# Kernel tuning notes

Measured on AMD Instinct MI355X. Metric: run time of the kernel, lower is better.

The kernel has to match this reference:

```python
import jax, jax.numpy as jnp
import numpy as np
from jax import lax

B, E, V, T = 16384, 256, 128, 16
TAU = 1.0


def _gru(x, h, Wih, Whh, bih, bhh):
    # torch.nn.GRUCell math
    gi = x @ Wih.T + bih
    gh = h @ Whh.T + bhh
    ir, iz, i_n = jnp.split(gi, 3, axis=-1)
    hr, hz, h_n = jnp.split(gh, 3, axis=-1)
    r = jax.nn.sigmoid(ir + hr)
    z = jax.nn.sigmoid(iz + hz)
    n = jnp.tanh(i_n + r * h_n)
    return (1.0 - z) * n + z * h


def setup_inputs() -> dict:
    key = jax.random.key(0)
    ks = jax.random.split(key, 10)
    s = 0.05
    w = lambda k, shape: jax.random.normal(k, shape, jnp.float32) * s
    return {
        "x": jax.random.normal(ks[0], (B, E), jnp.float32),
        "global_idxes": jnp.arange(B, dtype=jnp.int32),
        "uniform_noise": jax.random.uniform(ks[1], (T, B, V), dtype=jnp.float32),
        "dec_Wd2e": w(ks[2], (E, V)), "dec_bd2e": jnp.zeros((E,), jnp.float32),
        "dec_Wih": w(ks[3], (3 * E, E)), "dec_Whh": w(ks[4], (3 * E, E)),
        "dec_bih": jnp.zeros((3 * E,), jnp.float32), "dec_bhh": jnp.zeros((3 * E,), jnp.float32),
        "dec_We2d": w(ks[5], (V, E)), "dec_be2d": jnp.zeros((V,), jnp.float32),
        "enc_Wd2e": w(ks[6], (E, V)), "enc_bd2e": jnp.zeros((E,), jnp.float32),
        "enc_Wih": w(ks[7], (3 * E, E)), "enc_Whh": w(ks[8], (3 * E, E)),
        "enc_bih": jnp.zeros((3 * E,), jnp.float32), "enc_bhh": jnp.zeros((3 * E,), jnp.float32),
    }


def _forward(x, uniform_noise,
             dec_Wd2e, dec_bd2e, dec_Wih, dec_Whh, dec_bih, dec_bhh, dec_We2d, dec_be2d,
             enc_Wd2e, enc_bd2e, enc_Wih, enc_Whh, enc_bih, enc_bhh):
    Bn = x.shape[0]
    # gumbel noise from pre-sampled uniforms (deterministic)
    gnoise = -jnp.log(-jnp.log(uniform_noise + 1e-10) + 1e-10)  # [T,B,V]

    # ---- GumbelDecoder: sequential GRUCell decode with alive/dead masking ----
    def dec_step(carry, g_t):
        state, last_tok, alive, N, t = carry
        emb = last_tok @ dec_Wd2e.T + dec_bd2e
        state = _gru(emb, state, dec_Wih, dec_Whh, dec_bih, dec_bhh)
        logits = state @ dec_We2d.T + dec_be2d
        y_soft = jax.nn.softmax((logits + g_t) / TAU, axis=-1)
        idx = jnp.argmax(y_soft, axis=-1)
        y_hard = jax.nn.one_hot(idx, V, dtype=y_soft.dtype)
        # straight-through hard gumbel-softmax
        y = y_soft + lax.stop_gradient(y_hard - y_soft)
        ended = idx == 0  # token 0 is the terminator
        N = jnp.where(ended, jnp.minimum(N, t), N)
        alive = alive & (~ended)
        # dead rows (incl. newly ended) have their token zeroed, as in torch
        y = jnp.where(alive[:, None], y, 0.0)
        return (state, y, alive, N, t + 1), y

    init = (x, jnp.zeros((Bn, V), x.dtype), jnp.ones((Bn,), bool),
            jnp.full((Bn,), T, jnp.int32), jnp.int32(0))
    (_, _, _, N, _), utt = lax.scan(dec_step, init, gnoise)  # utt: [T,B,V]

    # ---- OnehotEncoder: sequential GRUCell encode with alive sieve (masked) ----
    def enc_step(carry, u_t):
        state, out_state, alive = carry
        emb = u_t @ enc_Wd2e.T + enc_bd2e
        state = _gru(emb, state, enc_Wih, enc_Whh, enc_bih, enc_bhh)
        out_state = jnp.where(alive[:, None], state, out_state)
        ended = u_t[:, 0] > 0.5  # terminator seen in utterance
        alive = alive & (~ended)
        return (state, out_state, alive), None

    z0 = jnp.zeros((Bn, E), x.dtype)
    (_, reconst, _), _ = lax.scan(enc_step, (z0, z0, jnp.ones((Bn,), bool)), utt)

    utterance = jnp.transpose(utt, (1, 0, 2))  # [B,T,V]
    return utterance, N, reconst


def reference(x, global_idxes, uniform_noise,
              dec_Wd2e, dec_bd2e, dec_Wih, dec_Whh, dec_bih, dec_bhh, dec_We2d, dec_be2d,
              enc_Wd2e, enc_bd2e, enc_Wih, enc_Whh, enc_bih, enc_bhh):
    del global_idxes  # unused by the original forward
    return _forward(x, uniform_noise,
                    dec_Wd2e, dec_bd2e, dec_Wih, dec_Whh, dec_bih, dec_bhh, dec_We2d, dec_be2d,
                    enc_Wd2e, enc_bd2e, enc_Wih, enc_Whh, enc_bih, enc_bhh)
```

## Files before the change

### kernel.cpp

```cpp
#include <hip/hip_runtime.h>


namespace {
constexpr int kB  = 16384;
constexpr int kE  = 256;
constexpr int kV  = 128;
constexpr int kT  = 16;
constexpr int kG3 = 768;

constexpr int kOffWdhhT  = 0;
constexpr int kOffWe2dT  = kG3 * kE;
constexpr int kOffDecTab = kOffWe2dT + kV * kE;
constexpr int kOffEncTab = kOffDecTab + 129 * kG3;
constexpr int kOffBTab   = kOffEncTab + 129 * kG3;
constexpr int kBCount    = 32 * kG3 * 8;
}

typedef short bf16x8 __attribute__((ext_vector_type(8)));
typedef float f32x4  __attribute__((ext_vector_type(4)));
typedef unsigned short u16;

__device__ __forceinline__ float sigmf(float v) { return 1.0f / (1.0f + expf(-v)); }
__device__ __forceinline__ float gumbelf(float u) {
  return -logf(-logf(u + 1e-10f) + 1e-10f);
}

__device__ __forceinline__ f32x4 mfma16(bf16x8 a, bf16x8 b, f32x4 c) {
  return __builtin_amdgcn_mfma_f32_16x16x32_bf16(a, b, c, 0, 0, 0);
}

struct Bf3 { bf16x8 h, m, l; };

__device__ __forceinline__ Bf3 split3(float4 a, float4 b) {
  const float v[8] = {a.x, a.y, a.z, a.w, b.x, b.y, b.z, b.w};
  union { bf16x8 b8; u16 u[8]; } H, M, L;
#pragma unroll
  for (int e = 0; e < 8; ++e) {
    const float f = v[e];
    const unsigned hb = __float_as_uint(f) & 0xffff0000u;
    const float f1 = f - __uint_as_float(hb);
    const unsigned mb = __float_as_uint(f1) & 0xffff0000u;
    const float f2 = f1 - __uint_as_float(mb);
    H.u[e] = (u16)(hb >> 16);
    M.u[e] = (u16)(mb >> 16);
    L.u[e] = (u16)(__float_as_uint(f2) >> 16);
  }
  Bf3 r; r.h = H.b8; r.m = M.b8; r.l = L.b8;
  return r;
}

__device__ __forceinline__ int hidx(int row, int col) {
  return row * kE + ((((col >> 3) ^ (row & 7)) << 3) | (col & 7));
}

__global__ void prep_transpose(const float* __restrict__ dWhh,
                               const float* __restrict__ We2d,
                               float* __restrict__ ws) {
  const int n1 = kG3 * kE;
  const int n2 = n1 + kV * kE;
  for (int i = blockIdx.x * blockDim.x + threadIdx.x; i < n2;
       i += gridDim.x * blockDim.x) {
    if (i < n1) {
      const int k = i / kG3, j = i - k * kG3;
      ws[i] = dWhh[j * kE + k];
    } else {
      const int t = i - n1;
      const int k = t / kV, v = t - k * kV;
      ws[i] = We2d[v * kE + k];
    }
  }
}

__global__ void prep_tables(const float* __restrict__ Wih,
                            const float* __restrict__ Wd2e,
                            const float* __restrict__ bd2e,
                            const float* __restrict__ bih,
                            float* __restrict__ tab) {
  const int i = blockIdx.x * blockDim.x + threadIdx.x;
  if (i >= 129 * kG3) return;
  const int v = i / kG3, j = i - v * kG3;
  const float* wr = Wih + j * kE;
  float acc = 0.0f;
  if (v < kV) {
    for (int k = 0; k < kE; ++k) acc = fmaf(wr[k], Wd2e[k * kV + v] + bd2e[k], acc);
  } else {
    for (int k = 0; k < kE; ++k) acc = fmaf(wr[k], bd2e[k], acc);
  }
  tab[i] = acc + bih[j];
}

__global__ void prep_bsplit(const float* __restrict__ eWhh,
                            u16* __restrict__ bt) {
  const int idx = blockIdx.x * blockDim.x + threadIdx.x;
  if (idx >= 32 * kG3) return;
  const int j = idx % kG3;
  const int kg = idx / kG3;
  u16* ph = bt + (size_t)idx * 8;
  u16* pm = ph + kBCount;
  u16* pl = pm + kBCount;
  const float* src = eWhh + j * kE + kg * 8;
#pragma unroll
  for (int e = 0; e < 8; ++e) {
    const float f = src[e];
    const unsigned hb = __float_as_uint(f) & 0xffff0000u;
    const float f1 = f - __uint_as_float(hb);
    const unsigned mb = __float_as_uint(f1) & 0xffff0000u;
    const float f2 = f1 - __uint_as_float(mb);
    ph[e] = (u16)(hb >> 16);
    pm[e] = (u16)(mb >> 16);
    pl[e] = (u16)(__float_as_uint(f2) >> 16);
  }
}

__device__ __forceinline__ void gru_half(float acc[8][3][4],
                                         const float (*__restrict__ h)[8],
                                         const float* __restrict__ WT,
                                         const int e0) {
#pragma unroll
  for (int r = 0; r < 8; ++r)
#pragma unroll
    for (int g = 0; g < 3; ++g)
#pragma unroll
      for (int c = 0; c < 4; ++c) acc[r][g][c] = 0.0f;
#pragma unroll 2
  for (int k = 0; k < kE; ++k) {
    const float4 hA = *(const float4*)(&h[k][0]);
    const float4 hB = *(const float4*)(&h[k][4]);
    const float* wp = WT + k * kG3 + e0;
    const float4 w0 = *(const float4*)(wp);
    const float4 w1 = *(const float4*)(wp + 256);
    const float4 w2 = *(const float4*)(wp + 512);
    const float hv[8] = {hA.x, hA.y, hA.z, hA.w, hB.x, hB.y, hB.z, hB.w};
    const float wv[3][4] = {{w0.x, w0.y, w0.z, w0.w},
                            {w1.x, w1.y, w1.z, w1.w},
                            {w2.x, w2.y, w2.z, w2.w}};
#pragma unroll
    for (int r = 0; r < 8; ++r)
#pragma unroll
      for (int g = 0; g < 3; ++g)
#pragma unroll
        for (int c = 0; c < 4; ++c)
          acc[r][g][c] = fmaf(hv[r], wv[g][c], acc[r][g][c]);
  }
}

__device__ __forceinline__ void gru_pointwise(float acc[8][3][4],
                                              float (*__restrict__ h)[8],
                                              const float* __restrict__ Tab,
                                              const int tok[8],
                                              const float4& br4, const float4& bz4,
                                              const float4& bn4, const int e0) {
  const float br[4] = {br4.x, br4.y, br4.z, br4.w};
  const float bz[4] = {bz4.x, bz4.y, bz4.z, bz4.w};
  const float bn[4] = {bn4.x, bn4.y, bn4.z, bn4.w};
#pragma unroll
  for (int r = 0; r < 8; ++r) {
    const float* gp = Tab + tok[r] * kG3 + e0;
    const float4 g0 = *(const float4*)(gp);
    const float4 g1 = *(const float4*)(gp + 256);
    const float4 g2 = *(const float4*)(gp + 512);
    const float gi[3][4] = {{g0.x, g0.y, g0.z, g0.w},
                            {g1.x, g1.y, g1.z, g1.w},
                            {g2.x, g2.y, g2.z, g2.w}};
#pragma unroll
    for (int c = 0; c < 4; ++c) {
      const float rg = sigmf(gi[0][c] + acc[r][0][c] + br[c]);
      const float zg = sigmf(gi[1][c] + acc[r][1][c] + bz[c]);
      const float ng = tanhf(gi[2][c] + rg * (acc[r][2][c] + bn[c]));
      acc[r][0][c] = ng;
      acc[r][1][c] = zg;
    }
  }
#pragma unroll
  for (int c = 0; c < 4; ++c) {
    const int e = e0 + c;
    const float4 hA = *(const float4*)(&h[e][0]);
    const float4 hB = *(const float4*)(&h[e][4]);
    const float ho[8] = {hA.x, hA.y, hA.z, hA.w, hB.x, hB.y, hB.z, hB.w};
    float hn[8];
#pragma unroll
    for (int r = 0; r < 8; ++r)
      hn[r] = (1.0f - acc[r][1][c]) * acc[r][0][c] + acc[r][1][c] * ho[r];
    *(float4*)(&h[e][0]) = make_float4(hn[0], hn[1], hn[2], hn[3]);
    *(float4*)(&h[e][4]) = make_float4(hn[4], hn[5], hn[6], hn[7]);
  }
}

__launch_bounds__(256, 2)
__global__ void gumbel_fused(const float* __restrict__ x,
                             const float* __restrict__ unoise,
                             const float* __restrict__ dbhh,
                             const float* __restrict__ dbe2d,
                             const float* __restrict__ ebhh,
                             const float* __restrict__ ws,
                             float* __restrict__ out) {
  const float* WdhhT  = ws + kOffWdhhT;
  const float* We2dT  = ws + kOffWe2dT;
  const float* DecTab = ws + kOffDecTab;
  const float* EncTab = ws + kOffEncTab;
  const u16* Bh_t = (const u16*)(ws + kOffBTab);
  const u16* Bm_t = Bh_t + kBCount;
  const u16* Bl_t = Bh_t + 2 * kBCount;

  __shared__ __align__(16) float hd_s[4][kE][8];
  __shared__ __align__(16) float henc[32 * kE];

  const int tid  = (int)threadIdx.x;
  const int w    = tid >> 6;
  const int jx   = tid & 63;
  const int brow0 = (int)blockIdx.x * 32;
  const int row0  = brow0 + w * 8;
  const int e0   = jx * 4;

  float (*hd)[8] = hd_s[w];

  for (int i = jx; i < kE * 8; i += 64) {
    const int r = i >> 8, k = i & (kE - 1);
    hd[k][r] = x[(size_t)(row0 + r) * kE + k];
  }
  for (int i = tid; i < 32 * kE; i += 256) henc[i] = 0.0f;
  __syncthreads();

  int tok[8], Nn[8];
  bool alive[8];
#pragma unroll
  for (int r = 0; r < 8; ++r) { tok[r] = kV; Nn[r] = kT; alive[r] = true; }

  const float4 dbr = *(const float4*)(dbhh + e0);
  const float4 dbz = *(const float4*)(dbhh + 256 + e0);
  const float4 dbn = *(const float4*)(dbhh + 512 + e0);
  const float2 be2 = *(const float2*)(dbe2d + 2 * jx);

  const int l15  = jx & 15;
  const int ksub = jx >> 4;
  const int arow0 = l15, arow1 = l15 + 16;
  const int a0base = arow0 * kE, a1base = arow1 * kE;
  const int a0m7 = arow0 & 7, a1m7 = arow1 & 7;
  float ebr[4], ebz[4], ebn[4];
#pragma unroll
  for (int nn = 0; nn < 4; ++nn) {
    const int ec = (w << 6) + (nn << 4) + l15;
    ebr[nn] = ebhh[ec];
    ebz[nn] = ebhh[kE + ec];
    ebn[nn] = ebhh[2 * kE + ec];
  }

  const size_t uttN = (size_t)kB * kT * kV;
  int* tokg = (int*)(out + uttN);

  float acc[8][3][4];
  const f32x4 zero4 = {0.0f, 0.0f, 0.0f, 0.0f};

  for (int t = 0; t < kT; ++t) {
    gru_half(acc, hd, WdhhT, e0);
    gru_pointwise(acc, hd, DecTab, tok, dbr, dbz, dbn, e0);
    __syncthreads();

    float l0[8], l1[8];
#pragma unroll
    for (int r = 0; r < 8; ++r) { l0[r] = 0.0f; l1[r] = 0.0f; }
#pragma unroll 2
    for (int k = 0; k < kE; ++k) {
      const float4 hA = *(const float4*)(&hd[k][0]);
      const float4 hB = *(const float4*)(&hd[k][4]);
      const float2 wv = *(const float2*)(We2dT + k * kV + 2 * jx);
      const float hv[8] = {hA.x, hA.y, hA.z, hA.w, hB.x, hB.y, hB.z, hB.w};
#pragma unroll
      for (int r = 0; r < 8; ++r) {
        l0[r] = fmaf(hv[r], wv.x, l0[r]);
        l1[r] = fmaf(hv[r], wv.y, l1[r]);
      }
    }
    const float* up = unoise + ((size_t)t * kB + row0) * kV + 2 * jx;
#pragma unroll
    for (int r = 0; r < 8; ++r) {
      const float2 u = *(const float2*)(up + (size_t)r * kV);
      const float a0 = l0[r] + be2.x + gumbelf(u.x);
      const float a1 = l1[r] + be2.y + gumbelf(u.y);
      float mv; int mi;
      if (a1 > a0) { mv = a1; mi = 2 * jx + 1; } else { mv = a0; mi = 2 * jx; }
#pragma unroll
      for (int off = 32; off >= 1; off >>= 1) {
        const float ov = __shfl_xor(mv, off, 64);
        const int   oi = __shfl_xor(mi, off, 64);
        if (ov > mv || (ov == mv && oi < mi)) { mv = ov; mi = oi; }
      }
      const bool ended = (mi == 0);
      if (ended) Nn[r] = (Nn[r] < t) ? Nn[r] : t;
      const bool anew = alive[r] && !ended;
      alive[r] = anew;
      tok[r] = anew ? mi : kV;
      if (jx == r) tokg[row0 + r] = tok[r];
      float2 pr;
      pr.x = (anew && mi == 2 * jx) ? 1.0f : 0.0f;
      pr.y = (anew && mi == 2 * jx + 1) ? 1.0f : 0.0f;
      *reinterpret_cast<float2*>(
          out + ((size_t)(row0 + r) * kT + t) * kV + 2 * jx) = pr;
    }

    f32x4 eacc[2][12];
#pragma unroll
    for (int m = 0; m < 2; ++m)
#pragma unroll
      for (int nt = 0; nt < 12; ++nt) eacc[m][nt] = zero4;

#pragma unroll 2
    for (int kt = 0; kt < 8; ++kt) {
      const int c0 = ((kt << 2) + ksub) ^ a0m7;
      const int c1 = ((kt << 2) + ksub) ^ a1m7;
      const float4 f00 = *(const float4*)&henc[a0base + (c0 << 3)];
      const float4 f01 = *(const float4*)&henc[a0base + (c0 << 3) + 4];
      const float4 f10 = *(const float4*)&henc[a1base + (c1 << 3)];
      const float4 f11 = *(const float4*)&henc[a1base + (c1 << 3) + 4];
      const Bf3 A0 = split3(f00, f01);
      const Bf3 A1 = split3(f10, f11);
      const int recb = (((kt << 2) + ksub) * kG3 + (w << 6) + l15) * 8;
#pragma unroll
      for (int nt = 0; nt < 12; ++nt) {
        const int off = recb + ((nt >> 2) * 256 + (nt & 3) * 16) * 8;
        const bf16x8 Bh = *reinterpret_cast<const bf16x8*>(Bh_t + off);
        const bf16x8 Bm = *reinterpret_cast<const bf16x8*>(Bm_t + off);
        const bf16x8 Bl = *reinterpret_cast<const bf16x8*>(Bl_t + off);
        eacc[0][nt] = mfma16(A0.h, Bh, eacc[0][nt]);
        eacc[1][nt] = mfma16(A1.h, Bh, eacc[1][nt]);
        eacc[0][nt] = mfma16(A0.h, Bm, eacc[0][nt]);
        eacc[1][nt] = mfma16(A1.h, Bm, eacc[1][nt]);
        eacc[0][nt] = mfma16(A0.m, Bh, eacc[0][nt]);
        eacc[1][nt] = mfma16(A1.m, Bh, eacc[1][nt]);
        eacc[0][nt] = mfma16(A0.h, Bl, eacc[0][nt]);
        eacc[1][nt] = mfma16(A1.h, Bl, eacc[1][nt]);
        eacc[0][nt] = mfma16(A0.l, Bh, eacc[0][nt]);
        eacc[1][nt] = mfma16(A1.l, Bh, eacc[1][nt]);
        eacc[0][nt] = mfma16(A0.m, Bm, eacc[0][nt]);
        eacc[1][nt] = mfma16(A1.m, Bm, eacc[1][nt]);
      }
    }
    __syncthreads();

#pragma unroll
    for (int m = 0; m < 2; ++m) {
#pragma unroll
      for (int j2 = 0; j2 < 4; ++j2) {
        const int row = (m << 4) + (ksub << 2) + j2;
        const int tk = tokg[brow0 + row];
        const float* gp = EncTab + tk * kG3;
#pragma unroll
        for (int nn = 0; nn < 4; ++nn) {
          const int ec = (w << 6) + (nn << 4) + l15;
          const float rg = sigmf(gp[ec] + eacc[m][nn][j2] + ebr[nn]);
          const float zg = sigmf(gp[kE + ec] + eacc[m][4 + nn][j2] + ebz[nn]);
          const float ng = tanhf(gp[2 * kE + ec] + rg * (eacc[m][8 + nn][j2] + ebn[nn]));
          const int hx = hidx(row, ec);
          const float ho = henc[hx];
          henc[hx] = (1.0f - zg) * ng + zg * ho;
        }
      }
    }
    __syncthreads();
  }

#pragma unroll
  for (int r = 0; r < 8; ++r)
    if (jx == r) out[uttN + row0 + r] = (float)Nn[r];
  for (int i = tid; i < 32 * kE; i += 256) {
    const int row = i >> 8, col = i & (kE - 1);
    out[uttN + kB + (size_t)(brow0 + row) * kE + col] = henc[hidx(row, col)];
  }
}

extern "C" void kernel_launch(void* const* d_in, const int* in_sizes, int n_in,
                              void* d_out, int out_size, void* d_ws, size_t ws_size,
                              hipStream_t stream) {
  (void)in_sizes; (void)n_in; (void)out_size; (void)ws_size;
  const float* x      = (const float*)d_in[0];
  const float* unoise = (const float*)d_in[2];
  const float* dWd2e  = (const float*)d_in[3];
  const float* dbd2e  = (const float*)d_in[4];
  const float* dWih   = (const float*)d_in[5];
  const float* dWhh   = (const float*)d_in[6];
  const float* dbih   = (const float*)d_in[7];
  const float* dbhh   = (const float*)d_in[8];
  const float* dWe2d  = (const float*)d_in[9];
  const float* dbe2d  = (const float*)d_in[10];
  const float* eWd2e  = (const float*)d_in[11];
  const float* ebd2e  = (const float*)d_in[12];
  const float* eWih   = (const float*)d_in[13];
  const float* eWhh   = (const float*)d_in[14];
  const float* ebih   = (const float*)d_in[15];
  const float* ebhh   = (const float*)d_in[16];
  float* ws = (float*)d_ws;

  prep_transpose<<<896, 256, 0, stream>>>(dWhh, dWe2d, ws);
  prep_tables<<<(129 * kG3 + 255) / 256, 256, 0, stream>>>(
      dWih, dWd2e, dbd2e, dbih, ws + kOffDecTab);
  prep_tables<<<(129 * kG3 + 255) / 256, 256, 0, stream>>>(
      eWih, eWd2e, ebd2e, ebih, ws + kOffEncTab);
  prep_bsplit<<<(32 * kG3 + 255) / 256, 256, 0, stream>>>(
      eWhh, (u16*)(ws + kOffBTab));
  gumbel_fused<<<kB / 32, 256, 0, stream>>>(
      x, unoise, dbhh, dbe2d, ebhh, ws, (float*)d_out);
}
```

Measured before the change: 3.630 ms.

## Double-buffer encoder MFMA weight fragment loads and drop a barrier

Restructures the encoder recurrent matmul into 32 groups and double-buffers the bf16 weight fragments in registers, so global loads for the next group are issued while MFMAs run on the current one. The first group's load is also hoisted ahead of the gumbel/argmax section. Alongside this, the __syncthreads after the decoder pointwise update is removed, the logits loop unroll is raised from 2 to 8, and the token is made wave-uniform with readfirstlane. The aim is to hide weight-load latency and cut barrier stalls, at the cost of higher register pressure. Dropping the barrier could cause a race on the shared hidden state unless gru_pointwise already synchronises.

Result: slower. 7.631 ms (+110.2%).

```diff
diff --git a/kernel.cpp b/kernel.cpp
--- a/kernel.cpp
+++ b/kernel.cpp
@@ -251,15 +251,63 @@
   float acc[8][3][4];
   const f32x4 zero4 = {0.0f, 0.0f, 0.0f, 0.0f};
 
+#define LOADG(buf, g)                                                         \
+  {                                                                           \
+    const int kt_ = (g) >> 2, sub_ = (g) & 3;                                 \
+    const int recb_ = (((kt_ << 2) + ksub) * kG3 + (w << 6) + l15) * 8;       \
+    _Pragma("unroll")                                                         \
+    for (int q = 0; q < 3; ++q) {                                             \
+      const int nt_ = sub_ * 3 + q;                                           \
+      const int off_ = recb_ + ((nt_ >> 2) * 256 + (nt_ & 3) * 16) * 8;       \
+      buf[q * 3 + 0] = *reinterpret_cast<const bf16x8*>(Bh_t + off_);         \
+      buf[q * 3 + 1] = *reinterpret_cast<const bf16x8*>(Bm_t + off_);         \
+      buf[q * 3 + 2] = *reinterpret_cast<const bf16x8*>(Bl_t + off_);         \
+    }                                                                         \
+  }
+
+#define AFRAG(kt_)                                                            \
+  {                                                                           \
+    const int c0_ = (((kt_) << 2) + ksub) ^ a0m7;                             \
+    const int c1_ = (((kt_) << 2) + ksub) ^ a1m7;                             \
+    const float4 f00 = *(const float4*)&henc[a0base + (c0_ << 3)];            \
+    const float4 f01 = *(const float4*)&henc[a0base + (c0_ << 3) + 4];        \
+    const float4 f10 = *(const float4*)&henc[a1base + (c1_ << 3)];            \
+    const float4 f11 = *(const float4*)&henc[a1base + (c1_ << 3) + 4];        \
+    A0 = split3(f00, f01);                                                    \
+    A1 = split3(f10, f11);                                                    \
+  }
+
+#define MFMAG(buf, g)                                                         \
+  {                                                                           \
+    _Pragma("unroll")                                                         \
+    for (int q = 0; q < 3; ++q) {                                             \
+      const int nt_ = ((g) & 3) * 3 + q;                                      \
+      const bf16x8 Bh = buf[q * 3 + 0];                                       \
+      const bf16x8 Bm = buf[q * 3 + 1];                                       \
+      const bf16x8 Bl = buf[q * 3 + 2];                                       \
+      eacc[0][nt_] = mfma16(A0.h, Bh, eacc[0][nt_]);                          \
+      eacc[1][nt_] = mfma16(A1.h, Bh, eacc[1][nt_]);                          \
+      eacc[0][nt_] = mfma16(A0.h, Bm, eacc[0][nt_]);                          \
+      eacc[1][nt_] = mfma16(A1.h, Bm, eacc[1][nt_]);                          \
+      eacc[0][nt_] = mfma16(A0.m, Bh, eacc[0][nt_]);                          \
+      eacc[1][nt_] = mfma16(A1.m, Bh, eacc[1][nt_]);                          \
+      eacc[0][nt_] = mfma16(A0.h, Bl, eacc[0][nt_]);                          \
+      eacc[1][nt_] = mfma16(A1.h, Bl, eacc[1][nt_]);                          \
+      eacc[0][nt_] = mfma16(A0.l, Bh, eacc[0][nt_]);                          \
+      eacc[1][nt_] = mfma16(A1.l, Bh, eacc[1][nt_]);                          \
+      eacc[0][nt_] = mfma16(A0.m, Bm, eacc[0][nt_]);                          \
+      eacc[1][nt_] = mfma16(A1.m, Bm, eacc[1][nt_]);                          \
+    }                                                                         \
+  }
+
   for (int t = 0; t < kT; ++t) {
     gru_half(acc, hd, WdhhT, e0);
     gru_pointwise(acc, hd, DecTab, tok, dbr, dbz, dbn, e0);
-    __syncthreads();
 
     float l0[8], l1[8];
 #pragma unroll
     for (int r = 0; r < 8; ++r) { l0[r] = 0.0f; l1[r] = 0.0f; }
-#pragma unroll 2
+#pragma unroll 8
     for (int k = 0; k < kE; ++k) {
       const float4 hA = *(const float4*)(&hd[k][0]);
       const float4 hB = *(const float4*)(&hd[k][4]);
@@ -271,6 +319,11 @@
         l1[r] = fmaf(hv[r], wv.y, l1[r]);
       }
     }
+
+    bf16x8 bufA[9], bufB[9];
+    Bf3 A0, A1;
+    LOADG(bufA, 0);
+
     const float* up = unoise + ((size_t)t * kB + row0) * kV + 2 * jx;
 #pragma unroll
     for (int r = 0; r < 8; ++r) {
@@ -289,7 +342,7 @@
       if (ended) Nn[r] = (Nn[r] < t) ? Nn[r] : t;
       const bool anew = alive[r] && !ended;
       alive[r] = anew;
-      tok[r] = anew ? mi : kV;
+      tok[r] = __builtin_amdgcn_readfirstlane(anew ? mi : kV);
       if (jx == r) tokg[row0 + r] = tok[r];
       float2 pr;
       pr.x = (anew && mi == 2 * jx) ? 1.0f : 0.0f;
@@ -303,37 +356,15 @@
     for (int m = 0; m < 2; ++m)
 #pragma unroll
       for (int nt = 0; nt < 12; ++nt) eacc[m][nt] = zero4;
-
-#pragma unroll 2
-    for (int kt = 0; kt < 8; ++kt) {
-      const int c0 = ((kt << 2) + ksub) ^ a0m7;
-      const int c1 = ((kt << 2) + ksub) ^ a1m7;
-      const float4 f00 = *(const float4*)&henc[a0base + (c0 << 3)];
-      const float4 f01 = *(const float4*)&henc[a0base + (c0 << 3) + 4];
-      const float4 f10 = *(const float4*)&henc[a1base + (c1 << 3)];
-      const float4 f11 = *(const float4*)&henc[a1base + (c1 << 3) + 4];
-      const Bf3 A0 = split3(f00, f01);
-      const Bf3 A1 = split3(f10, f11);
-      const int recb = (((kt << 2) + ksub) * kG3 + (w << 6) + l15) * 8;
-#pragma unroll
-      for (int nt = 0; nt < 12; ++nt) {
-        const int off = recb + ((nt >> 2) * 256 + (nt & 3) * 16) * 8;
-        const bf16x8 Bh = *reinterpret_cast<const bf16x8*>(Bh_t + off);
-        const bf16x8 Bm = *reinterpret_cast<const bf16x8*>(Bm_t + off);
-        const bf16x8 Bl = *reinterpret_cast<const bf16x8*>(Bl_t + off);
-        eacc[0][nt] = mfma16(A0.h, Bh, eacc[0][nt]);
-        eacc[1][nt] = mfma16(A1.h, Bh, eacc[1][nt]);
-        eacc[0][nt] = mfma16(A0.h, Bm, eacc[0][nt]);
-        eacc[1][nt] = mfma16(A1.h, Bm, eacc[1][nt]);
-        eacc[0][nt] = mfma16(A0.m, Bh, eacc[0][nt]);
-        eacc[1][nt] = mfma16(A1.m, Bh, eacc[1][nt]);
-        eacc[0][nt] = mfma16(A0.h, Bl, eacc[0][nt]);
-        eacc[1][nt] = mfma16(A1.h, Bl, eacc[1][nt]);
-        eacc[0][nt] = mfma16(A0.l, Bh, eacc[0][nt]);
-        eacc[1][nt] = mfma16(A1.l, Bh, eacc[1][nt]);
-        eacc[0][nt] = mfma16(A0.m, Bm, eacc[0][nt]);
-        eacc[1][nt] = mfma16(A1.m, Bm, eacc[1][nt]);
-      }
+    AFRAG(0);
+#pragma unroll
+    for (int gp = 0; gp < 16; ++gp) {
+      const int g0 = 2 * gp, g1 = g0 + 1;
+      LOADG(bufB, g1);
+      if ((g0 & 3) == 0 && g0 > 0) AFRAG(g0 >> 2);
+      MFMAG(bufA, g0);
+      if (gp < 15) LOADG(bufA, g0 + 2);
+      MFMAG(bufB, g1);
     }
     __syncthreads();
 
@@ -366,6 +397,9 @@
     const int row = i >> 8, col = i & (kE - 1);
     out[uttN + kB + (size_t)(brow0 + row) * kE + col] = henc[hidx(row, col)];
   }
+#undef LOADG
+#undef AFRAG
+#undef MFMAG
 }
 
 extern "C" void kernel_launch(void* const* d_in, const int* in_sizes, int n_in,
```

## Split fused decoder/encoder into separate kernels with token history buffer

Applied to the files above, without the earlier changes.

The single fused kernel, which interleaved the decoder GRU and the encoder GRU at each timestep, becomes two kernels. The decoder writes per-step tokens as bytes into a workspace history buffer, and the encoder kernel then runs over 16-row blocks with twice as many blocks and half the MFMA accumulators. The intent is to free registers and LDS in each kernel, raise occupancy and give the encoder more parallelism. In exchange it adds a kernel launch and a global round trip for tokens; it also unrolls the logits loop further and broadcasts tokens via readfirstlane.

Result: slower. 6.830 ms (+88.2%).

```diff
diff --git a/kernel.cpp b/kernel.cpp
--- a/kernel.cpp
+++ b/kernel.cpp
@@ -14,11 +14,13 @@
 constexpr int kOffEncTab = kOffDecTab + 129 * kG3;
 constexpr int kOffBTab   = kOffEncTab + 129 * kG3;
 constexpr int kBCount    = 32 * kG3 * 8;
+constexpr int kOffTok    = kOffBTab + (3 * kBCount) / 2;
 }
 
 typedef short bf16x8 __attribute__((ext_vector_type(8)));
 typedef float f32x4  __attribute__((ext_vector_type(4)));
 typedef unsigned short u16;
+typedef unsigned char u8;
 
 __device__ __forceinline__ float sigmf(float v) { return 1.0f / (1.0f + expf(-v)); }
 __device__ __forceinline__ float gumbelf(float u) {
@@ -112,104 +114,24 @@
   }
 }
 
-__device__ __forceinline__ void gru_half(float acc[8][3][4],
-                                         const float (*__restrict__ h)[8],
-                                         const float* __restrict__ WT,
-                                         const int e0) {
-#pragma unroll
-  for (int r = 0; r < 8; ++r)
-#pragma unroll
-    for (int g = 0; g < 3; ++g)
-#pragma unroll
-      for (int c = 0; c < 4; ++c) acc[r][g][c] = 0.0f;
-#pragma unroll 2
-  for (int k = 0; k < kE; ++k) {
-    const float4 hA = *(const float4*)(&h[k][0]);
-    const float4 hB = *(const float4*)(&h[k][4]);
-    const float* wp = WT + k * kG3 + e0;
-    const float4 w0 = *(const float4*)(wp);
-    const float4 w1 = *(const float4*)(wp + 256);
-    const float4 w2 = *(const float4*)(wp + 512);
-    const float hv[8] = {hA.x, hA.y, hA.z, hA.w, hB.x, hB.y, hB.z, hB.w};
-    const float wv[3][4] = {{w0.x, w0.y, w0.z, w0.w},
-                            {w1.x, w1.y, w1.z, w1.w},
-                            {w2.x, w2.y, w2.z, w2.w}};
-#pragma unroll
-    for (int r = 0; r < 8; ++r)
-#pragma unroll
-      for (int g = 0; g < 3; ++g)
-#pragma unroll
-        for (int c = 0; c < 4; ++c)
-          acc[r][g][c] = fmaf(hv[r], wv[g][c], acc[r][g][c]);
-  }
-}
-
-__device__ __forceinline__ void gru_pointwise(float acc[8][3][4],
-                                              float (*__restrict__ h)[8],
-                                              const float* __restrict__ Tab,
-                                              const int tok[8],
-                                              const float4& br4, const float4& bz4,
-                                              const float4& bn4, const int e0) {
-  const float br[4] = {br4.x, br4.y, br4.z, br4.w};
-  const float bz[4] = {bz4.x, bz4.y, bz4.z, bz4.w};
-  const float bn[4] = {bn4.x, bn4.y, bn4.z, bn4.w};
-#pragma unroll
-  for (int r = 0; r < 8; ++r) {
-    const float* gp = Tab + tok[r] * kG3 + e0;
-    const float4 g0 = *(const float4*)(gp);
-    const float4 g1 = *(const float4*)(gp + 256);
-    const float4 g2 = *(const float4*)(gp + 512);
-    const float gi[3][4] = {{g0.x, g0.y, g0.z, g0.w},
-                            {g1.x, g1.y, g1.z, g1.w},
-                            {g2.x, g2.y, g2.z, g2.w}};
-#pragma unroll
-    for (int c = 0; c < 4; ++c) {
-      const float rg = sigmf(gi[0][c] + acc[r][0][c] + br[c]);
-      const float zg = sigmf(gi[1][c] + acc[r][1][c] + bz[c]);
-      const float ng = tanhf(gi[2][c] + rg * (acc[r][2][c] + bn[c]));
-      acc[r][0][c] = ng;
-      acc[r][1][c] = zg;
-    }
-  }
-#pragma unroll
-  for (int c = 0; c < 4; ++c) {
-    const int e = e0 + c;
-    const float4 hA = *(const float4*)(&h[e][0]);
-    const float4 hB = *(const float4*)(&h[e][4]);
-    const float ho[8] = {hA.x, hA.y, hA.z, hA.w, hB.x, hB.y, hB.z, hB.w};
-    float hn[8];
-#pragma unroll
-    for (int r = 0; r < 8; ++r)
-      hn[r] = (1.0f - acc[r][1][c]) * acc[r][0][c] + acc[r][1][c] * ho[r];
-    *(float4*)(&h[e][0]) = make_float4(hn[0], hn[1], hn[2], hn[3]);
-    *(float4*)(&h[e][4]) = make_float4(hn[4], hn[5], hn[6], hn[7]);
-  }
-}
-
 __launch_bounds__(256, 2)
-__global__ void gumbel_fused(const float* __restrict__ x,
-                             const float* __restrict__ unoise,
-                             const float* __restrict__ dbhh,
-                             const float* __restrict__ dbe2d,
-                             const float* __restrict__ ebhh,
-                             const float* __restrict__ ws,
-                             float* __restrict__ out) {
+__global__ void dec_kernel(const float* __restrict__ x,
+                           const float* __restrict__ unoise,
+                           const float* __restrict__ dbhh,
+                           const float* __restrict__ dbe2d,
+                           const float* __restrict__ ws,
+                           u8* __restrict__ tokhist,
+                           float* __restrict__ out) {
   const float* WdhhT  = ws + kOffWdhhT;
   const float* We2dT  = ws + kOffWe2dT;
   const float* DecTab = ws + kOffDecTab;
-  const float* EncTab = ws + kOffEncTab;
-  const u16* Bh_t = (const u16*)(ws + kOffBTab);
-  const u16* Bm_t = Bh_t + kBCount;
-  const u16* Bl_t = Bh_t + 2 * kBCount;
 
   __shared__ __align__(16) float hd_s[4][kE][8];
-  __shared__ __align__(16) float henc[32 * kE];
 
   const int tid  = (int)threadIdx.x;
   const int w    = tid >> 6;
   const int jx   = tid & 63;
-  const int brow0 = (int)blockIdx.x * 32;
-  const int row0  = brow0 + w * 8;
+  const int row0 = (int)blockIdx.x * 32 + w * 8;
   const int e0   = jx * 4;
 
   float (*hd)[8] = hd_s[w];
@@ -218,8 +140,6 @@
     const int r = i >> 8, k = i & (kE - 1);
     hd[k][r] = x[(size_t)(row0 + r) * kE + k];
   }
-  for (int i = tid; i < 32 * kE; i += 256) henc[i] = 0.0f;
-  __syncthreads();
 
   int tok[8], Nn[8];
   bool alive[8];
@@ -231,35 +151,80 @@
   const float4 dbn = *(const float4*)(dbhh + 512 + e0);
   const float2 be2 = *(const float2*)(dbe2d + 2 * jx);
 
-  const int l15  = jx & 15;
-  const int ksub = jx >> 4;
-  const int arow0 = l15, arow1 = l15 + 16;
-  const int a0base = arow0 * kE, a1base = arow1 * kE;
-  const int a0m7 = arow0 & 7, a1m7 = arow1 & 7;
-  float ebr[4], ebz[4], ebn[4];
-#pragma unroll
-  for (int nn = 0; nn < 4; ++nn) {
-    const int ec = (w << 6) + (nn << 4) + l15;
-    ebr[nn] = ebhh[ec];
-    ebz[nn] = ebhh[kE + ec];
-    ebn[nn] = ebhh[2 * kE + ec];
-  }
-
   const size_t uttN = (size_t)kB * kT * kV;
-  int* tokg = (int*)(out + uttN);
-
   float acc[8][3][4];
-  const f32x4 zero4 = {0.0f, 0.0f, 0.0f, 0.0f};
 
   for (int t = 0; t < kT; ++t) {
-    gru_half(acc, hd, WdhhT, e0);
-    gru_pointwise(acc, hd, DecTab, tok, dbr, dbz, dbn, e0);
     __syncthreads();
 
+#pragma unroll
+    for (int r = 0; r < 8; ++r)
+#pragma unroll
+      for (int g = 0; g < 3; ++g)
+#pragma unroll
+        for (int c = 0; c < 4; ++c) acc[r][g][c] = 0.0f;
+#pragma unroll 2
+    for (int k = 0; k < kE; ++k) {
+      const float4 hA = *(const float4*)(&hd[k][0]);
+      const float4 hB = *(const float4*)(&hd[k][4]);
+      const float* wp = WdhhT + k * kG3 + e0;
+      const float4 w0 = *(const float4*)(wp);
+      const float4 w1 = *(const float4*)(wp + 256);
+      const float4 w2 = *(const float4*)(wp + 512);
+      const float hv[8] = {hA.x, hA.y, hA.z, hA.w, hB.x, hB.y, hB.z, hB.w};
+      const float wv[3][4] = {{w0.x, w0.y, w0.z, w0.w},
+                              {w1.x, w1.y, w1.z, w1.w},
+                              {w2.x, w2.y, w2.z, w2.w}};
+#pragma unroll
+      for (int r = 0; r < 8; ++r)
+#pragma unroll
+        for (int g = 0; g < 3; ++g)
+#pragma unroll
+          for (int c = 0; c < 4; ++c)
+            acc[r][g][c] = fmaf(hv[r], wv[g][c], acc[r][g][c]);
+    }
+
+    {
+      const float br[4] = {dbr.x, dbr.y, dbr.z, dbr.w};
+      const float bz[4] = {dbz.x, dbz.y, dbz.z, dbz.w};
+      const float bn[4] = {dbn.x, dbn.y, dbn.z, dbn.w};
+#pragma unroll
+      for (int r = 0; r < 8; ++r) {
+        const float* gp = DecTab + tok[r] * kG3 + e0;
+        const float4 g0 = *(const float4*)(gp);
+        const float4 g1 = *(const float4*)(gp + 256);
+        const float4 g2 = *(const float4*)(gp + 512);
+        const float gi[3][4] = {{g0.x, g0.y, g0.z, g0.w},
+                                {g1.x, g1.y, g1.z, g1.w},
+                                {g2.x, g2.y, g2.z, g2.w}};
+#pragma unroll
+        for (int c = 0; c < 4; ++c) {
+          const float rg = sigmf(gi[0][c] + acc[r][0][c] + br[c]);
+          const float zg = sigmf(gi[1][c] + acc[r][1][c] + bz[c]);
+          const float ng = tanhf(gi[2][c] + rg * (acc[r][2][c] + bn[c]));
+          acc[r][0][c] = ng;
+          acc[r][1][c] = zg;
+        }
+      }
+#pragma unroll
+      for (int c = 0; c < 4; ++c) {
+        const int e = e0 + c;
+        const float4 hA = *(const float4*)(&hd[e][0]);
+        const float4 hB = *(const float4*)(&hd[e][4]);
+        const float ho[8] = {hA.x, hA.y, hA.z, hA.w, hB.x, hB.y, hB.z, hB.w};
+        float hn[8];
+#pragma unroll
+        for (int r = 0; r < 8; ++r)
+          hn[r] = (1.0f - acc[r][1][c]) * acc[r][0][c] + acc[r][1][c] * ho[r];
+        *(float4*)(&hd[e][0]) = make_float4(hn[0], hn[1], hn[2], hn[3]);
+        *(float4*)(&hd[e][4]) = make_float4(hn[4], hn[5], hn[6], hn[7]);
+      }
+    }
+
     float l0[8], l1[8];
 #pragma unroll
     for (int r = 0; r < 8; ++r) { l0[r] = 0.0f; l1[r] = 0.0f; }
-#pragma unroll 2
+#pragma unroll 8
     for (int k = 0; k < kE; ++k) {
       const float4 hA = *(const float4*)(&hd[k][0]);
       const float4 hB = *(const float4*)(&hd[k][4]);
@@ -289,31 +254,68 @@
       if (ended) Nn[r] = (Nn[r] < t) ? Nn[r] : t;
       const bool anew = alive[r] && !ended;
       alive[r] = anew;
-      tok[r] = anew ? mi : kV;
-      if (jx == r) tokg[row0 + r] = tok[r];
+      tok[r] = __builtin_amdgcn_readfirstlane(anew ? mi : kV);
+      if (jx == r) tokhist[(size_t)t * kB + row0 + r] = (u8)tok[r];
       float2 pr;
       pr.x = (anew && mi == 2 * jx) ? 1.0f : 0.0f;
       pr.y = (anew && mi == 2 * jx + 1) ? 1.0f : 0.0f;
       *reinterpret_cast<float2*>(
           out + ((size_t)(row0 + r) * kT + t) * kV + 2 * jx) = pr;
     }
-
-    f32x4 eacc[2][12];
-#pragma unroll
-    for (int m = 0; m < 2; ++m)
-#pragma unroll
-      for (int nt = 0; nt < 12; ++nt) eacc[m][nt] = zero4;
-
-#pragma unroll 2
+  }
+
+#pragma unroll
+  for (int r = 0; r < 8; ++r)
+    if (jx == r) out[uttN + row0 + r] = (float)Nn[r];
+}
+
+__launch_bounds__(256, 2)
+__global__ void enc_kernel(const float* __restrict__ ebhh,
+                           const float* __restrict__ ws,
+                           const u8* __restrict__ tokhist,
+                           float* __restrict__ out) {
+  const float* EncTab = ws + kOffEncTab;
+  const u16* Bh_t = (const u16*)(ws + kOffBTab);
+  const u16* Bm_t = Bh_t + kBCount;
+  const u16* Bl_t = Bh_t + 2 * kBCount;
+
+  __shared__ __align__(16) float henc[16 * kE];
+
+  const int tid  = (int)threadIdx.x;
+  const int w    = tid >> 6;
+  const int jx   = tid & 63;
+  const int brow0 = (int)blockIdx.x * 16;
+
+  for (int i = tid; i < 16 * kE; i += 256) henc[i] = 0.0f;
+  __syncthreads();
+
+  const int l15  = jx & 15;
+  const int ksub = jx >> 4;
+  const int abase = l15 * kE;
+  const int am7 = l15 & 7;
+  float ebr[4], ebz[4], ebn[4];
+#pragma unroll
+  for (int nn = 0; nn < 4; ++nn) {
+    const int ec = (w << 6) + (nn << 4) + l15;
+    ebr[nn] = ebhh[ec];
+    ebz[nn] = ebhh[kE + ec];
+    ebn[nn] = ebhh[2 * kE + ec];
+  }
+
+  const size_t uttN = (size_t)kB * kT * kV;
+  const f32x4 zero4 = {0.0f, 0.0f, 0.0f, 0.0f};
+
+  for (int t = 0; t < kT; ++t) {
+    f32x4 eacc[12];
+#pragma unroll
+    for (int nt = 0; nt < 12; ++nt) eacc[nt] = zero4;
+
+#pragma unroll
     for (int kt = 0; kt < 8; ++kt) {
-      const int c0 = ((kt << 2) + ksub) ^ a0m7;
-      const int c1 = ((kt << 2) + ksub) ^ a1m7;
-      const float4 f00 = *(const float4*)&henc[a0base + (c0 << 3)];
-      const float4 f01 = *(const float4*)&henc[a0base + (c0 << 3) + 4];
-      const float4 f10 = *(const float4*)&henc[a1base + (c1 << 3)];
-      const float4 f11 = *(const float4*)&henc[a1base + (c1 << 3) + 4];
-      const Bf3 A0 = split3(f00, f01);
-      const Bf3 A1 = split3(f10, f11);
+      const int c0 = ((kt << 2) + ksub) ^ am7;
+      const float4 f00 = *(const float4*)&henc[abase + (c0 << 3)];
+      const float4 f01 = *(const float4*)&henc[abase + (c0 << 3) + 4];
+      const Bf3 A = split3(f00, f01);
       const int recb = (((kt << 2) + ksub) * kG3 + (w << 6) + l15) * 8;
 #pragma unroll
       for (int nt = 0; nt < 12; ++nt) {
@@ -321,48 +323,36 @@
         const bf16x8 Bh = *reinterpret_cast<const bf16x8*>(Bh_t + off);
         const bf16x8 Bm = *reinterpret_cast<const bf16x8*>(Bm_t + off);
         const bf16x8 Bl = *reinterpret_cast<const bf16x8*>(Bl_t + off);
-        eacc[0][nt] = mfma16(A0.h, Bh, eacc[0][nt]);
-        eacc[1][nt] = mfma16(A1.h, Bh, eacc[1][nt]);
-        eacc[0][nt] = mfma16(A0.h, Bm, eacc[0][nt]);
-        eacc[1][nt] = mfma16(A1.h, Bm, eacc[1][nt]);
-        eacc[0][nt] = mfma16(A0.m, Bh, eacc[0][nt]);
-        eacc[1][nt] = mfma16(A1.m, Bh, eacc[1][nt]);
-        eacc[0][nt] = mfma16(A0.h, Bl, eacc[0][nt]);
-        eacc[1][nt] = mfma16(A1.h, Bl, eacc[1][nt]);
-        eacc[0][nt] = mfma16(A0.l, Bh, eacc[0][nt]);
-        eacc[1][nt] = mfma16(A1.l, Bh, eacc[1][nt]);
-        eacc[0][nt] = mfma16(A0.m, Bm, eacc[0][nt]);
-        eacc[1][nt] = mfma16(A1.m, Bm, eacc[1][nt]);
+        eacc[nt] = mfma16(A.h, Bh, eacc[nt]);
+        eacc[nt] = mfma16(A.h, Bm, eacc[nt]);
+        eacc[nt] = mfma16(A.m, Bh, eacc[nt]);
+        eacc[nt] = mfma16(A.h, Bl, eacc[nt]);
+        eacc[nt] = mfma16(A.l, Bh, eacc[nt]);
+        eacc[nt] = mfma16(A.m, Bm, eacc[nt]);
       }
     }
     __syncthreads();
 
 #pragma unroll
-    for (int m = 0; m < 2; ++m) {
-#pragma unroll
-      for (int j2 = 0; j2 < 4; ++j2) {
-        const int row = (m << 4) + (ksub << 2) + j2;
-        const int tk = tokg[brow0 + row];
-        const float* gp = EncTab + tk * kG3;
-#pragma unroll
-        for (int nn = 0; nn < 4; ++nn) {
-          const int ec = (w << 6) + (nn << 4) + l15;
-          const float rg = sigmf(gp[ec] + eacc[m][nn][j2] + ebr[nn]);
-          const float zg = sigmf(gp[kE + ec] + eacc[m][4 + nn][j2] + ebz[nn]);
-          const float ng = tanhf(gp[2 * kE + ec] + rg * (eacc[m][8 + nn][j2] + ebn[nn]));
-          const int hx = hidx(row, ec);
-          const float ho = henc[hx];
-          henc[hx] = (1.0f - zg) * ng + zg * ho;
-        }
+    for (int j2 = 0; j2 < 4; ++j2) {
+      const int row = (ksub << 2) + j2;
+      const int tk = (int)tokhist[(size_t)t * kB + brow0 + row];
+      const float* gp = EncTab + tk * kG3;
+#pragma unroll
+      for (int nn = 0; nn < 4; ++nn) {
+        const int ec = (w << 6) + (nn << 4) + l15;
+        const float rg = sigmf(gp[ec] + eacc[nn][j2] + ebr[nn]);
+        const float zg = sigmf(gp[kE + ec] + eacc[4 + nn][j2] + ebz[nn]);
+        const float ng = tanhf(gp[2 * kE + ec] + rg * (eacc[8 + nn][j2] + ebn[nn]));
+        const int hx = hidx(row, ec);
+        const float ho = henc[hx];
+        henc[hx] = (1.0f - zg) * ng + zg * ho;
       }
     }
     __syncthreads();
   }
 
-#pragma unroll
-  for (int r = 0; r < 8; ++r)
-    if (jx == r) out[uttN + row0 + r] = (float)Nn[r];
-  for (int i = tid; i < 32 * kE; i += 256) {
+  for (int i = tid; i < 16 * kE; i += 256) {
     const int row = i >> 8, col = i & (kE - 1);
     out[uttN + kB + (size_t)(brow0 + row) * kE + col] = henc[hidx(row, col)];
   }
@@ -389,6 +379,7 @@
   const float* ebih   = (const float*)d_in[15];
   const float* ebhh   = (const float*)d_in[16];
   float* ws = (float*)d_ws;
+  u8* tokhist = (u8*)(ws + kOffTok);
 
   prep_transpose<<<896, 256, 0, stream>>>(dWhh, dWe2d, ws);
   prep_tables<<<(129 * kG3 + 255) / 256, 256, 0, stream>>>(
@@ -397,6 +388,8 @@
       eWih, eWd2e, ebd2e, ebih, ws + kOffEncTab);
   prep_bsplit<<<(32 * kG3 + 255) / 256, 256, 0, stream>>>(
       eWhh, (u16*)(ws + kOffBTab));
-  gumbel_fused<<<kB / 32, 256, 0, stream>>>(
-      x, unoise, dbhh, dbe2d, ebhh, ws, (float*)d_out);
-}
+  dec_kernel<<<kB / 32, 256, 0, stream>>>(
+      x, unoise, dbhh, dbe2d, ws, tokhist, (float*)d_out);
+  enc_kernel<<<kB / 16, 256, 0, stream>>>(
+      ebhh, ws, tokhist, (float*)d_out);
+}
```
